# Optimization experiments

Measured on AMD Instinct MI355X. Metric: run time of the kernel, lower is better.

The kernel has to match this reference:

```python
import jax, jax.numpy as jnp
import numpy as np

B, N, Q, D = 1, 6, 10000, 256
HEADS, LEVELS, NPTS, ZANCH = 8, 1, 8, 4  # NPTS = 2*n_points, ZANCH = num_points_in_pillar
HF, WF = 32, 88
HD = D // HEADS


def setup_inputs() -> dict:
    key = jax.random.key(0)
    ks = jax.random.split(key, 18)
    s = 1.0 / np.sqrt(D)
    inp = {
        'queries': jax.random.normal(ks[0], (B, N, Q, D), jnp.float32),
        'pos_emb': jax.random.normal(ks[1], (B, N, Q, D), jnp.float32),
        'lvl_emb': jax.random.normal(ks[2], (LEVELS, D), jnp.float32),
        'cam_emb': jax.random.normal(ks[3], (N, D), jnp.float32),
        'features0': jax.random.normal(ks[4], (B * N, D, HF, WF), jnp.float32),
        'reference_points_3D': jax.random.uniform(ks[5], (B, N, Q, ZANCH, 2), jnp.float32),
        'bev_mask': jax.random.randint(ks[6], (B, N, Q, ZANCH, 2), 0, 2).astype(bool),
        # MSDeformAttn3D params
        'W_value': jax.random.normal(ks[7], (D, D), jnp.float32) * s,
        'b_value': jnp.zeros((D,), jnp.float32),
        'W_off': jax.random.normal(ks[8], (HEADS * LEVELS * NPTS * 2, D), jnp.float32) * 0.01,
        'b_off': jax.random.uniform(ks[9], (HEADS * LEVELS * NPTS * 2,), jnp.float32, -2.0, 2.0),
        'W_attn': jax.random.normal(ks[10], (HEADS * LEVELS * NPTS, D), jnp.float32) * s,
        'b_attn': jnp.zeros((HEADS * LEVELS * NPTS,), jnp.float32),
        'W_inner': jax.random.normal(ks[11], (D, D), jnp.float32) * s,
        'b_inner': jnp.zeros((D,), jnp.float32),
        # SpatialCrossAttention.output_proj
        'W_out': jax.random.normal(ks[12], (D, D), jnp.float32) * s,
        'b_out': jnp.zeros((D,), jnp.float32),
    }
    return inp


def _bilinear(value_t, loc, H, W):
    # value_t: (bn, heads, H*W, hd); loc: (bn, q, heads, pts, 2) normalized to [0,1]
    bn, q, heads, pts, _ = loc.shape
    hd = value_t.shape[-1]
    # grid_sample(2*loc-1, align_corners=False) -> pixel coord = loc*size - 0.5
    x = loc[..., 0] * W - 0.5
    y = loc[..., 1] * H - 0.5
    x0 = jnp.floor(x); y0 = jnp.floor(y)
    dx = x - x0; dy = y - y0
    x0 = x0.astype(jnp.int32); y0 = y0.astype(jnp.int32)
    out = jnp.zeros((bn, heads, q * pts, hd), value_t.dtype)
    corners = ((0, 0, (1 - dx) * (1 - dy)), (1, 0, dx * (1 - dy)),
               (0, 1, (1 - dx) * dy), (1, 1, dx * dy))
    for ox, oy, w in corners:
        xi = x0 + ox; yi = y0 + oy
        valid = (xi >= 0) & (xi < W) & (yi >= 0) & (yi < H)  # zero padding
        wgt = jnp.where(valid, w, 0.0)
        idx = jnp.clip(yi, 0, H - 1) * W + jnp.clip(xi, 0, W - 1)  # (bn,q,heads,pts)
        idx_t = idx.transpose(0, 2, 1, 3).reshape(bn, heads, q * pts)
        g = jnp.take_along_axis(value_t, idx_t[..., None], axis=2)  # (bn,heads,q*pts,hd)
        wgt_t = wgt.transpose(0, 2, 1, 3).reshape(bn, heads, q * pts)
        out = out + g * wgt_t[..., None]
    return out.reshape(bn, heads, q, pts, hd)


def _forward(queries, pos_emb, lvl_emb, cam_emb, features0, reference_points_3D, bev_mask,
             W_value, b_value, W_off, b_off, W_attn, b_attn, W_inner, b_inner, W_out, b_out):
    b, n, q, d = queries.shape
    hf, wf = features0.shape[-2:]
    # flatten features + level/cam embeddings -> (b*n, hw, d)
    feat = features0.reshape(b, n, d, hf * wf)
    feat = feat + lvl_emb[0][None, None, :, None] + cam_emb[None, :, :, None]
    input_flatten = feat.transpose(0, 1, 3, 2).reshape(b * n, hf * wf, d)

    qp = (queries + pos_emb).reshape(b * n, q, d)
    ref = reference_points_3D.reshape(b * n, q, ZANCH, 2)

    # --- MSDeformAttn3D (single level) ---
    value = (input_flatten @ W_value.T + b_value).reshape(b * n, hf * wf, HEADS, HD)
    off = (qp @ W_off.T + b_off).reshape(b * n, q, HEADS, LEVELS, NPTS, 2)
    attw = jax.nn.softmax((qp @ W_attn.T + b_attn).reshape(b * n, q, HEADS, LEVELS * NPTS), axis=-1)
    attw = attw.reshape(b * n, q, HEADS, LEVELS, NPTS)
    normalizer = jnp.array([wf, hf], queries.dtype)  # (W, H)
    pts_per_z = NPTS // ZANCH
    off_z = off.reshape(b * n, q, HEADS, LEVELS, pts_per_z, ZANCH, 2)
    loc = ref[:, :, None, None, None, :, :] + off_z / normalizer
    loc = loc.reshape(b * n, q, HEADS, LEVELS, NPTS, 2)

    value_t = value.transpose(0, 2, 1, 3)  # (bn, heads, hw, hd)
    sampled = _bilinear(value_t, loc[:, :, :, 0], hf, wf)  # (bn,heads,q,pts,hd)
    attw_t = attw[:, :, :, 0].transpose(0, 2, 1, 3)  # (bn,heads,q,pts)
    out = jnp.einsum('bhqp,bhqpc->bqhc', attw_t, sampled).reshape(b * n, q, d)
    out = out @ W_inner.T + b_inner

    # --- scatter back per camera, normalize by hit count ---
    attn = out.reshape(b, n, q, d)
    # indexes come from batch 0's mask (as in the original code)
    hit = (bev_mask[0, :, :, :, 0].astype(jnp.int32).sum(-1) > 0).astype(queries.dtype)  # (n,q)
    slots = (attn * hit[None, :, :, None]).sum(1)  # (b,q,d)
    count = (bev_mask[..., 0].astype(jnp.int32).sum(-1) > 0).astype(queries.dtype).sum(1)
    count = jnp.clip(count, 1.0, None)  # (b,q)
    slots = slots / count[..., None]
    return slots @ W_out.T + b_out


def reference(queries, pos_emb, lvl_emb, cam_emb, features0, reference_points_3D, bev_mask,
              W_value, b_value, W_off, b_off, W_attn, b_attn, W_inner, b_inner, W_out, b_out):
    return _forward(queries, pos_emb, lvl_emb, cam_emb, features0, reference_points_3D, bev_mask,
                    W_value, b_value, W_off, b_off, W_attn, b_attn, W_inner, b_inner, W_out, b_out)
```

## Files before the change

### kernel.cpp

```cpp
#include <hip/hip_runtime.h>
#include <hip/hip_bf16.h>

#define BN     6
#define NQ     10000
#define DIM    256
#define HEADS  8
#define HDD    32
#define HF_    32
#define WF_    88
#define HW_    (HF_*WF_)
#define MTOT   (BN*NQ)

typedef __attribute__((ext_vector_type(8))) unsigned short ushort8_t;
typedef __attribute__((ext_vector_type(8))) short bf16x8;
typedef __attribute__((ext_vector_type(4))) float f32x4;

static __device__ inline unsigned short f2bf(float x) {
    __hip_bfloat16 b = __float2bfloat16(x);
    return *(unsigned short*)&b;
}

__global__ __launch_bounds__(256)
void k_prep(const float* __restrict__ Wv, const float* __restrict__ Wo,
            const float* __restrict__ Wa, const float* __restrict__ Wi,
            const float* __restrict__ Wz,
            const float* __restrict__ lvl, const float* __restrict__ cam,
            const float* __restrict__ bv, const int* __restrict__ bev,
            unsigned short* __restrict__ Wv_bf, unsigned short* __restrict__ Woa_bf,
            unsigned short* __restrict__ Wi_bf, unsigned short* __restrict__ Wz_bf,
            float* __restrict__ ebias, float* __restrict__ hitf,
            float* __restrict__ scale, float* __restrict__ biasf)
{
    const int b = blockIdx.x;
    const int tid = threadIdx.x;
    if (b < 64) {
        const int i4 = (b*256 + tid) * 4;
        if (i4 < 65536) {
            float4 v;
            ushort4 p;
            v = *(const float4*)(Wv+i4); p.x=f2bf(v.x);p.y=f2bf(v.y);p.z=f2bf(v.z);p.w=f2bf(v.w);
            *(ushort4*)(Wv_bf+i4) = p;
            v = *(const float4*)(Wi+i4); p.x=f2bf(v.x);p.y=f2bf(v.y);p.z=f2bf(v.z);p.w=f2bf(v.w);
            *(ushort4*)(Wi_bf+i4) = p;
            v = *(const float4*)(Wz+i4); p.x=f2bf(v.x);p.y=f2bf(v.y);p.z=f2bf(v.z);p.w=f2bf(v.w);
            *(ushort4*)(Wz_bf+i4) = p;
        }
        if (i4 < 32768) {
            float4 v = *(const float4*)(Wo+i4);
            ushort4 p; p.x=f2bf(v.x);p.y=f2bf(v.y);p.z=f2bf(v.z);p.w=f2bf(v.w);
            *(ushort4*)(Woa_bf+i4) = p;
        }
        if (i4 < 16384) {
            float4 v = *(const float4*)(Wa+i4);
            ushort4 p; p.x=f2bf(v.x);p.y=f2bf(v.y);p.z=f2bf(v.z);p.w=f2bf(v.w);
            *(ushort4*)(Woa_bf+32768+i4) = p;
        }
    } else if (b < 70) {
        const int n = b - 64;
        const int j = tid;
        __shared__ float e[DIM];
        e[j] = lvl[j] + cam[n*DIM + j];
        __syncthreads();
        const float* w = Wv + (size_t)j*DIM;
        float s = bv[j];
        for (int d = 0; d < DIM; ++d) s += e[d]*w[d];
        ebias[n*DIM + j] = s;
    } else {
        const int q = (b - 70)*256 + tid;
        if (q >= NQ) return;
        float cnt = 0.f;
        #pragma unroll
        for (int n = 0; n < BN; ++n) {
            int hit = 0;
            #pragma unroll
            for (int z = 0; z < 4; ++z)
                hit |= (bev[(((size_t)n*NQ + q)*4 + z)*2] != 0);
            hitf[(size_t)n*NQ + q] = (float)hit;
            cnt += (float)hit;
        }
        biasf[q] = (cnt > 0.f) ? 1.f : 0.f;
        scale[q] = 1.f / fmaxf(cnt, 1.f);
    }
}

__global__ __launch_bounds__(256)
void k_feat(const float* __restrict__ feat, unsigned short* __restrict__ featT)
{
    __shared__ float Tf[64][68];
    const int cam = blockIdx.z;
    const int d0 = blockIdx.y * 64;
    const int p0 = blockIdx.x * 64;
    const int tid = threadIdx.x;
    #pragma unroll
    for (int i = 0; i < 4; ++i) {
        const int d = (tid>>4) + i*16;
        const int p4 = (tid&15)*4;
        *(float4*)&Tf[d][p4] = *(const float4*)(feat + ((size_t)cam*DIM + d0 + d)*HW_ + p0 + p4);
    }
    __syncthreads();
    const int p = tid>>2, dq = tid&3;
    unsigned short* ob = featT + ((size_t)cam*HW_ + p0 + p)*DIM + d0;
    #pragma unroll
    for (int i = 0; i < 4; ++i) {
        const int d4 = dq*4 + i*16;
        ushort4 pk;
        pk.x = f2bf(Tf[d4+0][p]); pk.y = f2bf(Tf[d4+1][p]);
        pk.z = f2bf(Tf[d4+2][p]); pk.w = f2bf(Tf[d4+3][p]);
        *(ushort4*)(ob + d4) = pk;
    }
}

__global__ __launch_bounds__(256)
void k_value_mfma(const unsigned short* __restrict__ featT,
                  const unsigned short* __restrict__ Wv_bf,
                  const float* __restrict__ ebias,
                  unsigned short* __restrict__ value_bf)
{
    __shared__ unsigned short Ap[128][72];
    __shared__ unsigned short Bc[64][72];
    const int cam = blockIdx.z;
    const int p0 = blockIdx.x * 128;
    const int c0 = blockIdx.y * 64;
    const int tid = threadIdx.x;
    const int lane = tid & 63, wave = tid >> 6;
    const int quad = lane >> 4, l15 = lane & 15;
    f32x4 acc[2][4] = {};
    const unsigned short* fbase = featT + ((size_t)cam*HW_ + p0)*DIM;

    for (int k0 = 0; k0 < DIM; k0 += 64) {
        #pragma unroll
        for (int i = 0; i < 4; ++i) {
            const int row = (tid>>3) + i*32;
            const int k8 = (tid&7)*8;
            *(ushort8_t*)&Ap[row][k8] = *(const ushort8_t*)(fbase + (size_t)row*DIM + k0 + k8);
        }
        #pragma unroll
        for (int i = 0; i < 2; ++i) {
            const int row = (tid>>3) + i*32;
            const int k8 = (tid&7)*8;
            *(ushort8_t*)&Bc[row][k8] = *(const ushort8_t*)(Wv_bf + (size_t)(c0+row)*DIM + k0 + k8);
        }
        __syncthreads();
        #pragma unroll
        for (int s = 0; s < 2; ++s) {
            const int kf = s*32 + quad*8;
            bf16x8 a[2], b[4];
            #pragma unroll
            for (int mt = 0; mt < 2; ++mt)
                a[mt] = *(const bf16x8*)&Ap[(wave*2+mt)*16 + l15][kf];
            #pragma unroll
            for (int nt = 0; nt < 4; ++nt)
                b[nt] = *(const bf16x8*)&Bc[nt*16 + l15][kf];
            #pragma unroll
            for (int mt = 0; mt < 2; ++mt)
                #pragma unroll
                for (int nt = 0; nt < 4; ++nt)
                    acc[mt][nt] = __builtin_amdgcn_mfma_f32_16x16x32_bf16(a[mt], b[nt], acc[mt][nt], 0,0,0);
        }
        __syncthreads();
    }
    #pragma unroll
    for (int nt = 0; nt < 4; ++nt) {
        const int c = c0 + nt*16 + l15;
        const float eb = ebias[cam*DIM + c];
        const int h = c >> 5, cc = c & 31;
        unsigned short* vb = value_bf + (size_t)(cam*HEADS + h)*HW_*HDD + cc;
        #pragma unroll
        for (int mt = 0; mt < 2; ++mt)
            #pragma unroll
            for (int r = 0; r < 4; ++r) {
                const int p = p0 + (wave*2+mt)*16 + quad*4 + r;
                vb[(size_t)p*HDD] = f2bf(acc[mt][nt][r] + eb);
            }
    }
}

__global__ __launch_bounds__(256, 3)
void k_offattn(const float* __restrict__ Qr, const float* __restrict__ Pe,
               const unsigned short* __restrict__ Woa_bf,
               const float* __restrict__ boff, const float* __restrict__ battn,
               float* __restrict__ off_ws, float* __restrict__ attw_ws)
{
    __shared__ char smraw[32*204*4];
    unsigned short (*A_lds)[264] = (unsigned short (*)[264])smraw;
    float (*C_lds)[204] = (float (*)[204])smraw;

    const int m0 = blockIdx.x * 32;
    const int tid = threadIdx.x;
    const int lane = tid & 63, wave = tid >> 6;
    const int quad = lane >> 4, l15 = lane & 15;
    const int n0 = wave * 48;

    bf16x8 breg[3][8];
    #pragma unroll
    for (int nt = 0; nt < 3; ++nt) {
        const unsigned short* wb = Woa_bf + (size_t)(n0 + nt*16 + l15)*DIM + quad*8;
        #pragma unroll
        for (int kc = 0; kc < 8; ++kc)
            breg[nt][kc] = *(const bf16x8*)(wb + kc*32);
    }

    {
        const int row = tid >> 3;
        const int c8  = tid & 7;
        const float* qb = Qr + (size_t)(m0 + row)*DIM;
        const float* pb = Pe + (size_t)(m0 + row)*DIM;
        #pragma unroll
        for (int j = 0; j < 8; ++j) {
            const int col = c8*4 + j*32;
            const float4 x = *(const float4*)(qb + col);
            const float4 y = *(const float4*)(pb + col);
            ushort4 pk;
            pk.x = f2bf(x.x+y.x); pk.y = f2bf(x.y+y.y);
            pk.z = f2bf(x.z+y.z); pk.w = f2bf(x.w+y.w);
            *(ushort4*)&A_lds[row][col] = pk;
        }
    }
    __syncthreads();

    f32x4 acc[2][3] = {};
    #pragma unroll
    for (int kc = 0; kc < 8; ++kc) {
        const int kk = kc*32 + quad*8;
        const bf16x8 a0 = *(const bf16x8*)&A_lds[l15][kk];
        const bf16x8 a1 = *(const bf16x8*)&A_lds[16 + l15][kk];
        #pragma unroll
        for (int nt = 0; nt < 3; ++nt) {
            acc[0][nt] = __builtin_amdgcn_mfma_f32_16x16x32_bf16(a0, breg[nt][kc], acc[0][nt], 0,0,0);
            acc[1][nt] = __builtin_amdgcn_mfma_f32_16x16x32_bf16(a1, breg[nt][kc], acc[1][nt], 0,0,0);
        }
    }

    __syncthreads();
    #pragma unroll
    for (int nt = 0; nt < 3; ++nt) {
        const int col = n0 + nt*16 + l15;
        const float bias = (col < 128) ? boff[col] : battn[col-128];
        #pragma unroll
        for (int mt = 0; mt < 2; ++mt) {
            #pragma unroll
            for (int r = 0; r < 4; ++r)
                C_lds[mt*16 + quad*4 + r][col] = acc[mt][nt][r] + bias;
        }
    }
    __syncthreads();
    {
        float* a = &C_lds[tid>>3][128 + (tid&7)*8];
        float lg[8];
        float mx = -1e30f;
        #pragma unroll
        for (int p = 0; p < 8; ++p) { lg[p] = a[p]; mx = fmaxf(mx, lg[p]); }
        float ssum = 0.f;
        #pragma unroll
        for (int p = 0; p < 8; ++p) { lg[p] = __expf(lg[p]-mx); ssum += lg[p]; }
        const float inv = 1.f/ssum;
        #pragma unroll
        for (int p = 0; p < 8; ++p) a[p] = lg[p]*inv;
    }
    __syncthreads();
    #pragma unroll
    for (int i = 0; i < 4; ++i) {
        const int idx = i*256 + tid;
        const int row = idx >> 5, c4 = (idx & 31)*4;
        *(float4*)(off_ws + ((size_t)(m0+row))*128 + c4) = *(float4*)&C_lds[row][c4];
    }
    #pragma unroll
    for (int i = 0; i < 2; ++i) {
        const int idx = i*256 + tid;
        const int row = idx >> 4, c4 = (idx & 15)*4;
        *(float4*)(attw_ws + ((size_t)(m0+row))*64 + c4) = *(float4*)&C_lds[row][128 + c4];
    }
}

__global__ __launch_bounds__(256)
void k_sample(const unsigned short* __restrict__ value_bf,
              const float* __restrict__ off_ws, const float* __restrict__ attw_ws,
              const float* __restrict__ ref3d, const float* __restrict__ hitf,
              const float* __restrict__ scale, unsigned short* __restrict__ asum_bf)
{
    const int q0 = blockIdx.x * 8;
    const int tid = threadIdx.x;

    __shared__ float s_off[8][128];
    __shared__ float s_att[8][64];
    __shared__ float s_ref[8][8];
    __shared__ float s_hit[BN][8];
    __shared__ float s_scl[8];

    if (tid < 48) s_hit[tid>>3][tid&7] = hitf[(size_t)(tid>>3)*NQ + q0 + (tid&7)];
    if (tid < 8)  s_scl[tid] = scale[q0 + tid];

    const int quarter = tid & 3;
    const int h  = (tid >> 2) & 7;
    const int ql = tid >> 5;

    float acc[8];
    #pragma unroll
    for (int c = 0; c < 8; ++c) acc[c] = 0.f;

    for (int n = 0; n < BN; ++n) {
        __syncthreads();
        {
            const float4* so = (const float4*)(off_ws + ((size_t)n*NQ + q0)*128);
            ((float4*)&s_off[0][0])[tid] = so[tid];
            const float2* sa = (const float2*)(attw_ws + ((size_t)n*NQ + q0)*64);
            ((float2*)&s_att[0][0])[tid] = sa[tid];
            if (tid < 64)
                (&s_ref[0][0])[tid] = (ref3d + ((size_t)n*NQ + q0)*8)[tid];
        }
        __syncthreads();

        if (s_hit[n][ql] != 0.f) {
            const unsigned short* vbase =
                value_bf + (size_t)(n*HEADS + h)*HW_*HDD + quarter*8;

            #pragma unroll
            for (int p = 0; p < 8; ++p) {
                const int z = p & 3;
                const float wp = s_att[ql][h*8+p];
                const float ax = s_ref[ql][z*2+0]*WF_ + s_off[ql][h*16+p*2+0] - 0.5f;
                const float ay = s_ref[ql][z*2+1]*HF_ + s_off[ql][h*16+p*2+1] - 0.5f;
                const float fx = floorf(ax), fy = floorf(ay);
                const float dx = ax-fx, dy = ay-fy;
                const int x0 = (int)fx, y0 = (int)fy;
                #pragma unroll
                for (int oy = 0; oy < 2; ++oy) {
                    const int yi = y0 + oy;
                    const float wy = oy ? dy : 1.f-dy;
                    #pragma unroll
                    for (int ox = 0; ox < 2; ++ox) {
                        const int xi = x0 + ox;
                        const float wx = ox ? dx : 1.f-dx;
                        const bool valid = ((unsigned)xi < WF_) & ((unsigned)yi < HF_);
                        const float cw = valid ? wp*wy*wx : 0.f;
                        const int xc = min(max(xi, 0), WF_-1);
                        const int yc = min(max(yi, 0), HF_-1);
                        const ushort8_t v = *(const ushort8_t*)(vbase + (size_t)(yc*WF_ + xc)*HDD);
                        #pragma unroll
                        for (int c = 0; c < 8; ++c)
                            acc[c] += cw * __uint_as_float(((unsigned)v[c]) << 16);
                    }
                }
            }
        }
    }

    const float sc = s_scl[ql];
    ushort8_t o;
    #pragma unroll
    for (int c = 0; c < 8; ++c) o[c] = f2bf(acc[c]*sc);
    *(ushort8_t*)(asum_bf + ((size_t)(q0+ql))*DIM + h*HDD + quarter*8) = o;
}

__global__ __launch_bounds__(256)
void k_tail(const unsigned short* __restrict__ asum_bf,
            const unsigned short* __restrict__ Wi_bf,
            const unsigned short* __restrict__ Wz_bf,
            const float* __restrict__ bi, const float* __restrict__ bz,
            const float* __restrict__ biasf, float* __restrict__ out)
{
    __shared__ char smraw[32*260*4];
    unsigned short (*S_lds)[264] = (unsigned short (*)[264])smraw;
    float (*C_lds)[260] = (float (*)[260])smraw;

    const int m0 = blockIdx.x * 32;
    const int tid = threadIdx.x;
    const int lane = tid & 63, wave = tid >> 6;
    const int quad = lane >> 4, l15 = lane & 15;
    const int n0 = wave * 64;

    const int r0 = m0 + l15;
    const int r1 = m0 + 16 + l15;
    const unsigned short* a0p = asum_bf + (size_t)(r0 < NQ ? r0 : 0)*DIM;
    const unsigned short* a1p = asum_bf + (size_t)(r1 < NQ ? r1 : 0)*DIM;

    f32x4 acc[2][4] = {};
    #pragma unroll
    for (int kc = 0; kc < 8; ++kc) {
        const int kk = kc*32 + quad*8;
        const bf16x8 a0 = *(const bf16x8*)(a0p + kk);
        const bf16x8 a1 = *(const bf16x8*)(a1p + kk);
        #pragma unroll
        for (int nt = 0; nt < 4; ++nt) {
            const bf16x8 b = *(const bf16x8*)(Wi_bf + (size_t)(n0 + nt*16 + l15)*DIM + kk);
            acc[0][nt] = __builtin_amdgcn_mfma_f32_16x16x32_bf16(a0, b, acc[0][nt], 0,0,0);
            acc[1][nt] = __builtin_amdgcn_mfma_f32_16x16x32_bf16(a1, b, acc[1][nt], 0,0,0);
        }
    }
    #pragma unroll
    for (int nt = 0; nt < 4; ++nt) {
        const int col = n0 + nt*16 + l15;
        const float bj = bi[col];
        #pragma unroll
        for (int mt = 0; mt < 2; ++mt) {
            #pragma unroll
            for (int r = 0; r < 4; ++r) {
                const int m = m0 + mt*16 + quad*4 + r;
                const float f = (m < NQ) ? biasf[m] : 0.f;
                S_lds[mt*16 + quad*4 + r][col] = f2bf(acc[mt][nt][r] + f*bj);
            }
        }
    }
    __syncthreads();

    f32x4 acc2[2][4] = {};
    #pragma unroll
    for (int kc = 0; kc < 8; ++kc) {
        const int kk = kc*32 + quad*8;
        const bf16x8 s0 = *(const bf16x8*)&S_lds[l15][kk];
        const bf16x8 s1 = *(const bf16x8*)&S_lds[16 + l15][kk];
        #pragma unroll
        for (int nt = 0; nt < 4; ++nt) {
            const bf16x8 b = *(const bf16x8*)(Wz_bf + (size_t)(n0 + nt*16 + l15)*DIM + kk);
            acc2[0][nt] = __builtin_amdgcn_mfma_f32_16x16x32_bf16(s0, b, acc2[0][nt], 0,0,0);
            acc2[1][nt] = __builtin_amdgcn_mfma_f32_16x16x32_bf16(s1, b, acc2[1][nt], 0,0,0);
        }
    }
    __syncthreads();
    #pragma unroll
    for (int nt = 0; nt < 4; ++nt) {
        const int col = n0 + nt*16 + l15;
        const float bj = bz[col];
        #pragma unroll
        for (int mt = 0; mt < 2; ++mt) {
            #pragma unroll
            for (int r = 0; r < 4; ++r)
                C_lds[mt*16 + quad*4 + r][col] = acc2[mt][nt][r] + bj;
        }
    }
    __syncthreads();
    #pragma unroll
    for (int i = 0; i < 8; ++i) {
        const int idx = i*256 + tid;
        const int row = idx >> 6, c4 = (idx & 63)*4;
        const int m = m0 + row;
        if (m < NQ)
            *(float4*)(out + (size_t)m*DIM + c4) = *(float4*)&C_lds[row][c4];
    }
}

extern "C" void kernel_launch(void* const* d_in, const int* in_sizes, int n_in,
                              void* d_out, int out_size, void* d_ws, size_t ws_size,
                              hipStream_t stream)
{
    const float* queries = (const float*)d_in[0];
    const float* pos_emb = (const float*)d_in[1];
    const float* lvl_emb = (const float*)d_in[2];
    const float* cam_emb = (const float*)d_in[3];
    const float* features= (const float*)d_in[4];
    const float* ref3d   = (const float*)d_in[5];
    const int*   bev     = (const int*)d_in[6];
    const float* Wv = (const float*)d_in[7];
    const float* bv = (const float*)d_in[8];
    const float* Wo = (const float*)d_in[9];
    const float* bo = (const float*)d_in[10];
    const float* Wa = (const float*)d_in[11];
    const float* ba = (const float*)d_in[12];
    const float* Wi = (const float*)d_in[13];
    const float* bi = (const float*)d_in[14];
    const float* Wz = (const float*)d_in[15];
    const float* bz = (const float*)d_in[16];
    float* out = (float*)d_out;

    char* ws = (char*)d_ws;
    size_t o = 0;
    auto alloc = [&](size_t bytes) { char* p = ws + o; o += (bytes + 255) & ~size_t(255); return p; };
    unsigned short* value_bf = (unsigned short*)alloc((size_t)BN*HEADS*HW_*HDD*2);
    unsigned short* featT    = (unsigned short*)alloc((size_t)BN*HW_*DIM*2);
    float* off_ws   = (float*)alloc((size_t)MTOT*128*4);
    float* attw_ws  = (float*)alloc((size_t)MTOT*64*4);
    unsigned short* asum_bf  = (unsigned short*)alloc((size_t)NQ*DIM*2);
    unsigned short* Wv_bf  = (unsigned short*)alloc(65536*2);
    unsigned short* Woa_bf = (unsigned short*)alloc(49152*2);
    unsigned short* Wi_bf  = (unsigned short*)alloc(65536*2);
    unsigned short* Wz_bf  = (unsigned short*)alloc(65536*2);
    float* hitf   = (float*)alloc((size_t)BN*NQ*4);
    float* scalev = (float*)alloc(NQ*4);
    float* biasf  = (float*)alloc(NQ*4);
    float* ebias  = (float*)alloc(BN*DIM*4);

    k_prep  <<<110, 256, 0, stream>>>(Wv, Wo, Wa, Wi, Wz, lvl_emb, cam_emb, bv, bev,
                                      Wv_bf, Woa_bf, Wi_bf, Wz_bf,
                                      ebias, hitf, scalev, biasf);
    k_feat  <<<dim3(HW_/64, DIM/64, BN), 256, 0, stream>>>(features, featT);
    k_value_mfma<<<dim3(HW_/128, DIM/64, BN), 256, 0, stream>>>(featT, Wv_bf, ebias, value_bf);
    k_offattn<<<MTOT/32, 256, 0, stream>>>(queries, pos_emb, Woa_bf, bo, ba, off_ws, attw_ws);
    k_sample <<<NQ/8, 256, 0, stream>>>(value_bf, off_ws, attw_ws, ref3d, hitf, scalev, asum_bf);
    k_tail   <<<(NQ+31)/32, 256, 0, stream>>>(asum_bf, Wi_bf, Wz_bf, bi, bz, biasf, out);
}
```

Before: 325.8 us.

## Retile value projection to full-width rows with LDS-staged coalesced stores; split ebias dot

The value projection GEMM now gives each block 16 pixels across all 256 output channels. It loads A and B fragments straight from global memory instead of staging K-chunks through LDS, and writes results through an LDS tile so the per-head value layout is stored as 16-byte coalesced vectors rather than scattered 2-byte writes. The ebias computation in the prep kernel is split across four times more blocks, with a 4-way partial-dot reduction, to shorten the serial 256-length loop. The trade-off is more global and L2 reads of weights per block and no LDS reuse of the weight tile.

```diff
diff --git a/kernel.cpp b/kernel.cpp
--- a/kernel.cpp
+++ b/kernel.cpp
@@ -55,18 +55,28 @@
             ushort4 p; p.x=f2bf(v.x);p.y=f2bf(v.y);p.z=f2bf(v.z);p.w=f2bf(v.w);
             *(ushort4*)(Woa_bf+32768+i4) = p;
         }
-    } else if (b < 70) {
-        const int n = b - 64;
-        const int j = tid;
+    } else if (b < 88) {
+        const int idx = b - 64;
+        const int n  = idx >> 2;
+        const int jq = idx & 3;
         __shared__ float e[DIM];
-        e[j] = lvl[j] + cam[n*DIM + j];
+        __shared__ float red[64][5];
+        e[tid] = lvl[tid] + cam[n*DIM + tid];
         __syncthreads();
-        const float* w = Wv + (size_t)j*DIM;
-        float s = bv[j];
-        for (int d = 0; d < DIM; ++d) s += e[d]*w[d];
-        ebias[n*DIM + j] = s;
+        const int j  = jq*64 + (tid >> 2);
+        const int dq = tid & 3;
+        const float* w  = Wv + (size_t)j*DIM + dq*64;
+        const float* ee = e + dq*64;
+        float s = 0.f;
+        #pragma unroll
+        for (int i = 0; i < 64; ++i) s += ee[i]*w[i];
+        red[tid>>2][dq] = s;
+        __syncthreads();
+        if (dq == 0)
+            ebias[n*DIM + j] = bv[j] + red[tid>>2][0] + red[tid>>2][1]
+                                     + red[tid>>2][2] + red[tid>>2][3];
     } else {
-        const int q = (b - 70)*256 + tid;
+        const int q = (b - 88)*256 + tid;
         if (q >= NQ) return;
         float cnt = 0.f;
         #pragma unroll
@@ -116,62 +126,46 @@
                   const float* __restrict__ ebias,
                   unsigned short* __restrict__ value_bf)
 {
-    __shared__ unsigned short Ap[128][72];
-    __shared__ unsigned short Bc[64][72];
+    __shared__ unsigned short C_lds[16][264];
     const int cam = blockIdx.z;
-    const int p0 = blockIdx.x * 128;
-    const int c0 = blockIdx.y * 64;
+    const int p0 = blockIdx.x * 16;
     const int tid = threadIdx.x;
     const int lane = tid & 63, wave = tid >> 6;
     const int quad = lane >> 4, l15 = lane & 15;
-    f32x4 acc[2][4] = {};
-    const unsigned short* fbase = featT + ((size_t)cam*HW_ + p0)*DIM;
-
-    for (int k0 = 0; k0 < DIM; k0 += 64) {
-        #pragma unroll
-        for (int i = 0; i < 4; ++i) {
-            const int row = (tid>>3) + i*32;
-            const int k8 = (tid&7)*8;
-            *(ushort8_t*)&Ap[row][k8] = *(const ushort8_t*)(fbase + (size_t)row*DIM + k0 + k8);
-        }
-        #pragma unroll
-        for (int i = 0; i < 2; ++i) {
-            const int row = (tid>>3) + i*32;
-            const int k8 = (tid&7)*8;
-            *(ushort8_t*)&Bc[row][k8] = *(const ushort8_t*)(Wv_bf + (size_t)(c0+row)*DIM + k0 + k8);
-        }
-        __syncthreads();
-        #pragma unroll
-        for (int s = 0; s < 2; ++s) {
-            const int kf = s*32 + quad*8;
-            bf16x8 a[2], b[4];
-            #pragma unroll
-            for (int mt = 0; mt < 2; ++mt)
-                a[mt] = *(const bf16x8*)&Ap[(wave*2+mt)*16 + l15][kf];
-            #pragma unroll
-            for (int nt = 0; nt < 4; ++nt)
-                b[nt] = *(const bf16x8*)&Bc[nt*16 + l15][kf];
-            #pragma unroll
-            for (int mt = 0; mt < 2; ++mt)
-                #pragma unroll
-                for (int nt = 0; nt < 4; ++nt)
-                    acc[mt][nt] = __builtin_amdgcn_mfma_f32_16x16x32_bf16(a[mt], b[nt], acc[mt][nt], 0,0,0);
-        }
-        __syncthreads();
-    }
+    const int n0 = wave * 64;
+
+    const unsigned short* abase = featT + ((size_t)cam*HW_ + p0 + l15)*DIM;
+    f32x4 acc[4] = {};
+
+    #pragma unroll
+    for (int kc = 0; kc < 8; ++kc) {
+        const int kk = kc*32 + quad*8;
+        const bf16x8 a = *(const bf16x8*)(abase + kk);
+        #pragma unroll
+        for (int nt = 0; nt < 4; ++nt) {
+            const bf16x8 bfr = *(const bf16x8*)(Wv_bf + (size_t)(n0 + nt*16 + l15)*DIM + kk);
+            acc[nt] = __builtin_amdgcn_mfma_f32_16x16x32_bf16(a, bfr, acc[nt], 0,0,0);
+        }
+    }
+
     #pragma unroll
     for (int nt = 0; nt < 4; ++nt) {
-        const int c = c0 + nt*16 + l15;
-        const float eb = ebias[cam*DIM + c];
-        const int h = c >> 5, cc = c & 31;
-        unsigned short* vb = value_bf + (size_t)(cam*HEADS + h)*HW_*HDD + cc;
-        #pragma unroll
-        for (int mt = 0; mt < 2; ++mt)
-            #pragma unroll
-            for (int r = 0; r < 4; ++r) {
-                const int p = p0 + (wave*2+mt)*16 + quad*4 + r;
-                vb[(size_t)p*HDD] = f2bf(acc[mt][nt][r] + eb);
-            }
+        const int col = n0 + nt*16 + l15;
+        const float eb = ebias[cam*DIM + col];
+        #pragma unroll
+        for (int r = 0; r < 4; ++r)
+            C_lds[quad*4 + r][col] = f2bf(acc[nt][r] + eb);
+    }
+    __syncthreads();
+    #pragma unroll
+    for (int i = 0; i < 2; ++i) {
+        const int idx = i*256 + tid;
+        const int p = idx >> 5;
+        const int seg = idx & 31;
+        const int h = seg >> 2, part = seg & 3;
+        unsigned short* dst = value_bf +
+            ((size_t)(cam*HEADS + h)*HW_ + p0 + p)*HDD + part*8;
+        *(ushort8_t*)dst = *(const ushort8_t*)&C_lds[p][h*32 + part*8];
     }
 }
 
@@ -479,11 +473,11 @@
     float* biasf  = (float*)alloc(NQ*4);
     float* ebias  = (float*)alloc(BN*DIM*4);
 
-    k_prep  <<<110, 256, 0, stream>>>(Wv, Wo, Wa, Wi, Wz, lvl_emb, cam_emb, bv, bev,
+    k_prep  <<<128, 256, 0, stream>>>(Wv, Wo, Wa, Wi, Wz, lvl_emb, cam_emb, bv, bev,
                                       Wv_bf, Woa_bf, Wi_bf, Wz_bf,
                                       ebias, hitf, scalev, biasf);
     k_feat  <<<dim3(HW_/64, DIM/64, BN), 256, 0, stream>>>(features, featT);
-    k_value_mfma<<<dim3(HW_/128, DIM/64, BN), 256, 0, stream>>>(featT, Wv_bf, ebias, value_bf);
+    k_value_mfma<<<dim3(HW_/16, 1, BN), 256, 0, stream>>>(featT, Wv_bf, ebias, value_bf);
     k_offattn<<<MTOT/32, 256, 0, stream>>>(queries, pos_emb, Woa_bf, bo, ba, off_ws, attw_ws);
     k_sample <<<NQ/8, 256, 0, stream>>>(value_bf, off_ws, attw_ws, ref3d, hitf, scalev, asum_bf);
     k_tail   <<<(NQ+31)/32, 256, 0, stream>>>(asum_bf, Wi_bf, Wz_bf, bi, bz, biasf, out);
```

Result: no change. 331.3 us (+1.7%).
